# Performance work log

Measured on AMD Instinct MI355X. Metric: run time of the kernel, lower is better.

The kernel has to match this reference:

```python
import jax, jax.numpy as jnp
import numpy as np

B, S, D = 8, 2048, 512
H, LAT, OUT = 8, 64, 64


def setup_inputs() -> dict:
    key = jax.random.key(0)
    ks = jax.random.split(key, 5)
    return {
        "x": jax.random.normal(ks[0], (B, S, D), dtype=jnp.float32),
        "WQ": jax.random.normal(ks[1], (H, D, LAT), dtype=jnp.float32) * 0.05,
        "WK": jax.random.normal(ks[2], (H, D, LAT), dtype=jnp.float32) * 0.05,
        "WV": jax.random.normal(ks[3], (H, D, OUT), dtype=jnp.float32) * 0.05,
        "WO": jax.random.normal(ks[4], (H * OUT, OUT), dtype=jnp.float32) * 0.05,
    }


def reference(x, WQ, WK, WV, WO):
    # Per-head projections, vectorized over heads (faithful to the TF python loop).
    Q = jnp.einsum('bsd,hdk->bhsk', x, WQ)   # [B,H,S,LAT]
    K = jnp.einsum('bsd,hdk->bhsk', x, WK)   # [B,H,S,LAT]
    V = jnp.einsum('bsd,hdo->bhso', x, WV)   # [B,H,S,OUT]
    scale = jnp.asarray(1.0 / np.sqrt(LAT), dtype=x.dtype)
    A = jnp.einsum('bhqk,bhsk->bhqs', Q, K) * scale  # [B,H,S,S]
    A = jax.nn.softmax(A, axis=-1)
    O = jnp.einsum('bhqs,bhso->bhqo', A, V)  # [B,H,S,OUT]
    # concat heads along last axis (head 0 first, matching the TF loop order)
    O = jnp.transpose(O, (0, 2, 1, 3)).reshape(x.shape[0], x.shape[1], H * OUT)
    return O @ WO  # [B,S,OUT]
```

## Files before the change

kernel.cpp:

```cpp
#include <hip/hip_runtime.h>
#include <hip/hip_bf16.h>
#include <math.h>

static constexpr int Bn = 8, Sn = 2048, Dn = 512, Hn = 8, LATn = 64, OUTn = 64;

typedef short  bf16x8 __attribute__((ext_vector_type(8)));
typedef float  f32x4  __attribute__((ext_vector_type(4)));

__device__ __forceinline__ unsigned short f2bf(float f) {
    union { float f; unsigned int i; } v; v.f = f;
    unsigned int x = v.i;
    return (unsigned short)((x + 0x7FFFu + ((x >> 16) & 1u)) >> 16);
}
__device__ __forceinline__ unsigned int pack2bf(float a, float b) {
    unsigned int ua = __float_as_uint(a) + 0x8000u;
    unsigned int ub = __float_as_uint(b) + 0x8000u;
    return (ua >> 16) | (ub & 0xFFFF0000u);
}
__device__ __forceinline__ unsigned int cvtpk(float a, float b) {
    unsigned int r;
    asm("v_cvt_pk_bf16_f32 %0, %1, %2" : "=v"(r) : "v"(a), "v"(b));
    return r;
}

#if __has_builtin(__builtin_amdgcn_exp2f)
#define EXP2(x) __builtin_amdgcn_exp2f(x)
#else
#define EXP2(x) exp2f(x)
#endif

__device__ __forceinline__ void gl_lds16(const void* g, void* l) {
    __builtin_amdgcn_global_load_lds(
        (const __attribute__((address_space(1))) unsigned int*)g,
        (__attribute__((address_space(3))) unsigned int*)l, 16, 0, 0);
}

__global__ __launch_bounds__(256) void wprep(
    const float* __restrict__ WQ, const float* __restrict__ WK,
    const float* __restrict__ WV, const float* __restrict__ WO,
    unsigned short* __restrict__ WT)
{
    __shared__ float tile[64][65];
    const int t  = threadIdx.x;
    const int d0 = blockIdx.x * 64;
    const int yy = blockIdx.y;

    const float* W; float scale = 1.0f; size_t dstbase;
    if (yy < 24) {
        int h = yy / 3, which = yy % 3;
        W = (which == 0) ? WQ : (which == 1) ? WK : WV;
        W += (size_t)h * Dn * 64;
        if (which == 0) scale = 0.125f * 1.44269504088896f;
        dstbase = ((size_t)h * 192 + which * 64) * Dn;
    } else {
        W = WO;
        dstbase = (size_t)8 * 192 * Dn;
    }

    for (int i = 0; i < 4; ++i) {
        int idx = i * 256 + t;
        int r = idx >> 4, c = (idx & 15) * 4;
        float4 u = *(const float4*)(W + (size_t)(d0 + r) * 64 + c);
        tile[r][c] = u.x; tile[r][c+1] = u.y; tile[r][c+2] = u.z; tile[r][c+3] = u.w;
    }
    __syncthreads();
    const int n = t & 63, dd = t >> 6;
    unsigned short pk[16];
    for (int i = 0; i < 16; ++i) pk[i] = f2bf(tile[dd*16 + i][n] * scale);
    size_t dst = dstbase + (size_t)n * Dn + d0 + dd * 16;
    *(bf16x8*)(WT + dst)     = *(bf16x8*)(pk);
    *(bf16x8*)(WT + dst + 8) = *(bf16x8*)(pk + 8);
}

__global__ __launch_bounds__(256) void qkv_mfma(
    const float* __restrict__ x, const unsigned short* __restrict__ WT,
    unsigned short* __restrict__ Qb, unsigned short* __restrict__ Kb,
    unsigned short* __restrict__ VT)
{
    __shared__ __align__(16) unsigned short lds[64*72 + 192*72];
    unsigned short* Xs = lds;
    unsigned short* Ws = lds + 64*72;
    unsigned short* L  = lds;

    const int t  = threadIdx.x;
    const int w  = t >> 6, ln = t & 63;
    const int nl = ln & 15, g = ln >> 4;
    const int bh = blockIdx.y, b = bh >> 3, h = bh & 7;
    const int s0 = blockIdx.x * 64;

    f32x4 acc[4][3];
    for (int m = 0; m < 4; ++m)
        for (int j = 0; j < 3; ++j) acc[m][j] = (f32x4){0.f, 0.f, 0.f, 0.f};

    for (int k0 = 0; k0 < Dn; k0 += 64) {
        __syncthreads();
        for (int i = 0; i < 2; ++i) {
            int idx = i * 256 + t;
            int r = idx >> 3, c = (idx & 7) * 8;
            const float* src = x + ((size_t)(b * Sn + s0 + r)) * Dn + k0 + c;
            float4 u0 = *(const float4*)(src);
            float4 u1 = *(const float4*)(src + 4);
            unsigned int pk[4] = { pack2bf(u0.x, u0.y), pack2bf(u0.z, u0.w),
                                   pack2bf(u1.x, u1.y), pack2bf(u1.z, u1.w) };
            *(bf16x8*)(Xs + r*72 + c) = *(bf16x8*)pk;
        }
        for (int i = 0; i < 6; ++i) {
            int idx = i * 256 + t;
            int r = idx >> 3, c = (idx & 7) * 8;
            *(bf16x8*)(Ws + r*72 + c) =
                *(const bf16x8*)(WT + ((size_t)h * 192 + r) * Dn + k0 + c);
        }
        __syncthreads();
        #pragma unroll
        for (int kc = 0; kc < 2; ++kc) {
            bf16x8 a[4], bb[3];
            for (int m = 0; m < 4; ++m)
                a[m]  = *(const bf16x8*)(Xs + (16*m + nl)*72 + 32*kc + 8*g);
            for (int j = 0; j < 3; ++j)
                bb[j] = *(const bf16x8*)(Ws + ((3*w + j)*16 + nl)*72 + 32*kc + 8*g);
            for (int m = 0; m < 4; ++m)
                for (int j = 0; j < 3; ++j)
                    acc[m][j] = __builtin_amdgcn_mfma_f32_16x16x32_bf16(
                                    a[m], bb[j], acc[m][j], 0, 0, 0);
        }
    }
    __syncthreads();
    for (int m = 0; m < 4; ++m)
        for (int j = 0; j < 3; ++j) {
            int n = 48*w + 16*j + nl;
            for (int r = 0; r < 4; ++r)
                L[(16*m + 4*g + r)*200 + n] = f2bf(acc[m][j][r]);
        }
    __syncthreads();
    for (int i = 0; i < 4; ++i) {
        int idx = i * 256 + t;
        int r = idx >> 4, c = (idx & 15) * 8;
        bf16x8 v = *(const bf16x8*)(L + r*200 + c);
        size_t o = ((size_t)bh * Sn + s0 + r) * 64;
        if (c < 64) *(bf16x8*)(Qb + o + c)      = v;
        else        *(bf16x8*)(Kb + o + c - 64) = v;
    }
    {
        int o = t & 63, cc = t >> 6;
        unsigned short pk[16];
        for (int i = 0; i < 16; ++i) {
            int srow = 32*(cc>>1) + 16*((i>>2)&1) + 8*(cc&1) + 4*((i>>3)&1) + (i&3);
            pk[i] = L[srow*200 + 128 + o];
        }
        size_t dst = ((size_t)bh * 64 + o) * Sn + s0 + 16*cc;
        *(bf16x8*)(VT + dst)     = *(bf16x8*)(pk);
        *(bf16x8*)(VT + dst + 8) = *(bf16x8*)(pk + 8);
    }
}

__global__ __launch_bounds__(256, 2) void flash_mfma(
    const unsigned short* __restrict__ Qb,
    const unsigned short* __restrict__ Kb,
    const unsigned short* __restrict__ VT,
    unsigned short* __restrict__ Ob)
{
    __shared__ __align__(16) unsigned short KV[3][2][4096];

    const int t  = threadIdx.x;
    const int w  = t >> 6, ln = t & 63;
    const int qh = ln & 15, g = (ln >> 4) & 3;
    const int bh = blockIdx.y, b = bh >> 3, h = bh & 7;
    const int q0 = blockIdx.x * 256;
    const int qw = q0 + 64 * w;

    bf16x8 bq[4][2];
    #pragma unroll
    for (int qs = 0; qs < 4; ++qs) {
        const unsigned short* qp =
            Qb + ((size_t)bh * Sn + qw + 16*qs + qh) * 64 + 8*g;
        bq[qs][0] = *(const bf16x8*)(qp);
        bq[qs][1] = *(const bf16x8*)(qp + 32);
    }

    const int r0a = t >> 3;
    const int csa = (t & 7) ^ (r0a & 7);
    const int r0b = 32 + (t >> 3);
    const int csb = (t & 7) ^ (r0b & 7);
    const unsigned short* kga = Kb + ((size_t)bh * Sn + r0a) * 64 + csa * 8;
    const unsigned short* kgb = Kb + ((size_t)bh * Sn + r0b) * 64 + csb * 8;
    const unsigned short* vga = VT + ((size_t)bh * 64 + r0a) * Sn + csa * 8;
    const unsigned short* vgb = VT + ((size_t)bh * 64 + r0b) * Sn + csb * 8;

    const int koff0 = qh*64 + (((g    ) ^ (qh & 7)) * 8);
    const int koff1 = qh*64 + (((4 + g) ^ (qh & 7)) * 8);

    f32x4 o_acc[4][4];
    #pragma unroll
    for (int qs = 0; qs < 4; ++qs)
        #pragma unroll
        for (int f = 0; f < 4; ++f) o_acc[qs][f] = (f32x4){0.f, 0.f, 0.f, 0.f};
    float l_run[4] = {0.f, 0.f, 0.f, 0.f};

    gl_lds16(kga,        &KV[0][0][w * 512]);
    gl_lds16(kgb,        &KV[0][0][2048 + w * 512]);
    gl_lds16(vga,        &KV[0][1][w * 512]);
    gl_lds16(vgb,        &KV[0][1][2048 + w * 512]);
    gl_lds16(kga + 4096, &KV[1][0][w * 512]);
    gl_lds16(kgb + 4096, &KV[1][0][2048 + w * 512]);
    gl_lds16(vga + 64,   &KV[1][1][w * 512]);
    gl_lds16(vgb + 64,   &KV[1][1][2048 + w * 512]);

    constexpr int NT = Sn / 64;
    int buf = 0, sbuf = 2;
    for (int kt = 0; kt < NT; ++kt) {
        if (kt < NT - 1) asm volatile("s_waitcnt vmcnt(4)" ::: "memory");
        else             asm volatile("s_waitcnt vmcnt(0)" ::: "memory");
        __builtin_amdgcn_s_barrier();

        if (kt < NT - 2) {
            const size_t ko = (size_t)(kt + 2) * 4096;
            const int    vo = (kt + 2) * 64;
            gl_lds16(kga + ko, &KV[sbuf][0][w * 512]);
            gl_lds16(kgb + ko, &KV[sbuf][0][2048 + w * 512]);
            gl_lds16(vga + vo, &KV[sbuf][1][w * 512]);
            gl_lds16(vgb + vo, &KV[sbuf][1][2048 + w * 512]);
        }
        const unsigned short* Kt = KV[buf][0];
        const unsigned short* Vt = KV[buf][1];

        f32x4 st[4][4];
        #pragma unroll
        for (int qs = 0; qs < 4; ++qs)
            #pragma unroll
            for (int f = 0; f < 4; ++f) st[qs][f] = (f32x4){0.f, 0.f, 0.f, 0.f};
        __builtin_amdgcn_s_setprio(1);
        #pragma unroll
        for (int kc = 0; kc < 2; ++kc) {
            const int ko = kc ? koff1 : koff0;
            bf16x8 a0 = *(const bf16x8*)(Kt + ko);
            bf16x8 a1 = *(const bf16x8*)(Kt + ko + 1024);
            bf16x8 a2 = *(const bf16x8*)(Kt + ko + 2048);
            bf16x8 a3 = *(const bf16x8*)(Kt + ko + 3072);
            #pragma unroll
            for (int qs = 0; qs < 4; ++qs) {
                st[qs][0] = __builtin_amdgcn_mfma_f32_16x16x32_bf16(a0, bq[qs][kc], st[qs][0], 0, 0, 0);
                st[qs][1] = __builtin_amdgcn_mfma_f32_16x16x32_bf16(a1, bq[qs][kc], st[qs][1], 0, 0, 0);
                st[qs][2] = __builtin_amdgcn_mfma_f32_16x16x32_bf16(a2, bq[qs][kc], st[qs][2], 0, 0, 0);
                st[qs][3] = __builtin_amdgcn_mfma_f32_16x16x32_bf16(a3, bq[qs][kc], st[qs][3], 0, 0, 0);
            }
        }
        __builtin_amdgcn_s_setprio(0);

        bf16x8 bp[4][2];
        #pragma unroll
        for (int qs = 0; qs < 4; ++qs) {
            float e0[4], e1[4], e2[4], e3[4];
            #pragma unroll
            for (int r = 0; r < 4; ++r) {
                e0[r] = EXP2(st[qs][0][r]);
                e1[r] = EXP2(st[qs][1][r]);
                e2[r] = EXP2(st[qs][2][r]);
                e3[r] = EXP2(st[qs][3][r]);
            }
            l_run[qs] += ((e0[0]+e0[1])+(e0[2]+e0[3])) + ((e1[0]+e1[1])+(e1[2]+e1[3]))
                       + ((e2[0]+e2[1])+(e2[2]+e2[3])) + ((e3[0]+e3[1])+(e3[2]+e3[3]));
            unsigned int p0[4] = { cvtpk(e0[0],e0[1]), cvtpk(e0[2],e0[3]),
                                   cvtpk(e1[0],e1[1]), cvtpk(e1[2],e1[3]) };
            unsigned int p1[4] = { cvtpk(e2[0],e2[1]), cvtpk(e2[2],e2[3]),
                                   cvtpk(e3[0],e3[1]), cvtpk(e3[2],e3[3]) };
            bp[qs][0] = *(bf16x8*)p0;
            bp[qs][1] = *(bf16x8*)p1;
        }

        __builtin_amdgcn_s_setprio(1);
        #pragma unroll
        for (int kc = 0; kc < 2; ++kc) {
            const int ko = kc ? koff1 : koff0;
            bf16x8 v0 = *(const bf16x8*)(Vt + ko);
            bf16x8 v1 = *(const bf16x8*)(Vt + ko + 1024);
            bf16x8 v2 = *(const bf16x8*)(Vt + ko + 2048);
            bf16x8 v3 = *(const bf16x8*)(Vt + ko + 3072);
            #pragma unroll
            for (int qs = 0; qs < 4; ++qs) {
                o_acc[qs][0] = __builtin_amdgcn_mfma_f32_16x16x32_bf16(v0, bp[qs][kc], o_acc[qs][0], 0, 0, 0);
                o_acc[qs][1] = __builtin_amdgcn_mfma_f32_16x16x32_bf16(v1, bp[qs][kc], o_acc[qs][1], 0, 0, 0);
                o_acc[qs][2] = __builtin_amdgcn_mfma_f32_16x16x32_bf16(v2, bp[qs][kc], o_acc[qs][2], 0, 0, 0);
                o_acc[qs][3] = __builtin_amdgcn_mfma_f32_16x16x32_bf16(v3, bp[qs][kc], o_acc[qs][3], 0, 0, 0);
            }
        }
        __builtin_amdgcn_s_setprio(0);

        buf  = (buf  == 2) ? 0 : buf  + 1;
        sbuf = (sbuf == 2) ? 0 : sbuf + 1;
    }

    #pragma unroll
    for (int qs = 0; qs < 4; ++qs) {
        l_run[qs] += __shfl_xor(l_run[qs], 16);
        l_run[qs] += __shfl_xor(l_run[qs], 32);
    }

    #pragma unroll
    for (int qs = 0; qs < 4; ++qs) {
        float inv_l = 1.f / l_run[qs];
        unsigned short* op = Ob
            + ((size_t)(b * Sn + q0 + 64*w + 16*qs + qh)) * 512 + h*64 + 4*g;
        #pragma unroll
        for (int f = 0; f < 4; ++f) {
            unsigned int lo = cvtpk(o_acc[qs][f][0] * inv_l, o_acc[qs][f][1] * inv_l);
            unsigned int hi = cvtpk(o_acc[qs][f][2] * inv_l, o_acc[qs][f][3] * inv_l);
            *(uint2*)(op + 16*f) = make_uint2(lo, hi);
        }
    }
}

__global__ __launch_bounds__(256) void out_mfma(
    const unsigned short* __restrict__ Ob, const unsigned short* __restrict__ WOT,
    float* __restrict__ out)
{
    __shared__ __align__(16) unsigned short As[64 * 72];
    __shared__ __align__(16) unsigned short Bs[64 * 72];

    const int t  = threadIdx.x;
    const int w  = t >> 6, ln = t & 63;
    const int qh = ln & 15, g = ln >> 4;
    const int bs0 = blockIdx.x * 64;

    f32x4 acc[4];
    for (int n = 0; n < 4; ++n) acc[n] = (f32x4){0.f, 0.f, 0.f, 0.f};

    for (int k0 = 0; k0 < 512; k0 += 64) {
        __syncthreads();
        for (int i = 0; i < 2; ++i) {
            int idx = i * 256 + t;
            int r = idx >> 3, c = (idx & 7) * 8;
            *(bf16x8*)(As + r*72 + c) =
                *(const bf16x8*)(Ob + ((size_t)(bs0 + r)) * 512 + k0 + c);
            *(bf16x8*)(Bs + r*72 + c) =
                *(const bf16x8*)(WOT + (size_t)r * Dn + k0 + c);
        }
        __syncthreads();
        #pragma unroll
        for (int kc = 0; kc < 2; ++kc) {
            bf16x8 a = *(const bf16x8*)(As + (16*w + qh)*72 + 32*kc + 8*g);
            #pragma unroll
            for (int n = 0; n < 4; ++n) {
                bf16x8 bb = *(const bf16x8*)(Bs + (16*n + qh)*72 + 32*kc + 8*g);
                acc[n] = __builtin_amdgcn_mfma_f32_16x16x32_bf16(a, bb, acc[n], 0, 0, 0);
            }
        }
    }
    for (int n = 0; n < 4; ++n)
        for (int r = 0; r < 4; ++r)
            out[((size_t)(bs0 + 16*w + 4*g + r)) * 64 + 16*n + qh] = acc[n][r];
}

extern "C" void kernel_launch(void* const* d_in, const int* in_sizes, int n_in,
                              void* d_out, int out_size, void* d_ws, size_t ws_size,
                              hipStream_t stream)
{
    const float* x  = (const float*)d_in[0];
    const float* WQ = (const float*)d_in[1];
    const float* WK = (const float*)d_in[2];
    const float* WV = (const float*)d_in[3];
    const float* WO = (const float*)d_in[4];
    float* out = (float*)d_out;

    const size_t NQ = (size_t)Bn * Hn * Sn * LATn;
    char* p = (char*)d_ws;
    unsigned short* Qb  = (unsigned short*)p;           p += NQ * 2;
    unsigned short* Kb  = (unsigned short*)p;           p += NQ * 2;
    unsigned short* VT  = (unsigned short*)p;           p += NQ * 2;
    unsigned short* WT  = (unsigned short*)p;           p += ((size_t)Hn*192*Dn + 64*Dn) * 2;
    unsigned short* Ob  = (unsigned short*)p;
    unsigned short* WOT = WT + (size_t)Hn * 192 * Dn;

    wprep     <<<dim3(8, 25),         256, 0, stream>>>(WQ, WK, WV, WO, WT);
    qkv_mfma  <<<dim3(Sn/64, Bn*Hn),  256, 0, stream>>>(x, WT, Qb, Kb, VT);
    flash_mfma<<<dim3(Sn/256, Bn*Hn), 256, 0, stream>>>(Qb, Kb, VT, Ob);
    out_mfma  <<<dim3(Bn*Sn/64),      256, 0, stream>>>(Ob, WOT, out);
}
```

Baseline: 208.4 us.

## Split flash attention block into 8 waves of 32 query rows each

The flash attention kernel now launches 512 threads per block instead of 256, and each wave handles 32 query rows instead of 64. The block still covers 256 queries. Each thread now issues one K and one V global-to-LDS load per tile rather than two of each, and the waitcnt values are adjusted to match. The intent is to lower per-wave register pressure and raise the number of resident waves for better latency hiding. In exchange, each wave reuses every LDS K/V fragment read across fewer MFMAs, and barrier synchronisation now spans more waves.

```diff
diff --git a/kernel.cpp b/kernel.cpp
--- a/kernel.cpp
+++ b/kernel.cpp
@@ -153,7 +153,7 @@
     }
 }
 
-__global__ __launch_bounds__(256, 2) void flash_mfma(
+__global__ __launch_bounds__(512, 4) void flash_mfma(
     const unsigned short* __restrict__ Qb,
     const unsigned short* __restrict__ Kb,
     const unsigned short* __restrict__ VT,
@@ -166,66 +166,54 @@
     const int qh = ln & 15, g = (ln >> 4) & 3;
     const int bh = blockIdx.y, b = bh >> 3, h = bh & 7;
     const int q0 = blockIdx.x * 256;
-    const int qw = q0 + 64 * w;
-
-    bf16x8 bq[4][2];
+    const int qw = q0 + 32 * w;
+
+    bf16x8 bq[2][2];
     #pragma unroll
-    for (int qs = 0; qs < 4; ++qs) {
+    for (int qs = 0; qs < 2; ++qs) {
         const unsigned short* qp =
             Qb + ((size_t)bh * Sn + qw + 16*qs + qh) * 64 + 8*g;
         bq[qs][0] = *(const bf16x8*)(qp);
         bq[qs][1] = *(const bf16x8*)(qp + 32);
     }
 
-    const int r0a = t >> 3;
-    const int csa = (t & 7) ^ (r0a & 7);
-    const int r0b = 32 + (t >> 3);
-    const int csb = (t & 7) ^ (r0b & 7);
-    const unsigned short* kga = Kb + ((size_t)bh * Sn + r0a) * 64 + csa * 8;
-    const unsigned short* kgb = Kb + ((size_t)bh * Sn + r0b) * 64 + csb * 8;
-    const unsigned short* vga = VT + ((size_t)bh * 64 + r0a) * Sn + csa * 8;
-    const unsigned short* vgb = VT + ((size_t)bh * 64 + r0b) * Sn + csb * 8;
+    const int r0 = t >> 3;
+    const int cs = (t & 7) ^ (r0 & 7);
+    const unsigned short* kg = Kb + ((size_t)bh * Sn + r0) * 64 + cs * 8;
+    const unsigned short* vg = VT + ((size_t)bh * 64 + r0) * Sn + cs * 8;
 
     const int koff0 = qh*64 + (((g    ) ^ (qh & 7)) * 8);
     const int koff1 = qh*64 + (((4 + g) ^ (qh & 7)) * 8);
 
-    f32x4 o_acc[4][4];
+    f32x4 o_acc[2][4];
     #pragma unroll
-    for (int qs = 0; qs < 4; ++qs)
+    for (int qs = 0; qs < 2; ++qs)
         #pragma unroll
         for (int f = 0; f < 4; ++f) o_acc[qs][f] = (f32x4){0.f, 0.f, 0.f, 0.f};
-    float l_run[4] = {0.f, 0.f, 0.f, 0.f};
-
-    gl_lds16(kga,        &KV[0][0][w * 512]);
-    gl_lds16(kgb,        &KV[0][0][2048 + w * 512]);
-    gl_lds16(vga,        &KV[0][1][w * 512]);
-    gl_lds16(vgb,        &KV[0][1][2048 + w * 512]);
-    gl_lds16(kga + 4096, &KV[1][0][w * 512]);
-    gl_lds16(kgb + 4096, &KV[1][0][2048 + w * 512]);
-    gl_lds16(vga + 64,   &KV[1][1][w * 512]);
-    gl_lds16(vgb + 64,   &KV[1][1][2048 + w * 512]);
+    float l_run[2] = {0.f, 0.f};
+
+    gl_lds16(kg,        &KV[0][0][w * 512]);
+    gl_lds16(vg,        &KV[0][1][w * 512]);
+    gl_lds16(kg + 4096, &KV[1][0][w * 512]);
+    gl_lds16(vg + 64,   &KV[1][1][w * 512]);
 
     constexpr int NT = Sn / 64;
     int buf = 0, sbuf = 2;
     for (int kt = 0; kt < NT; ++kt) {
-        if (kt < NT - 1) asm volatile("s_waitcnt vmcnt(4)" ::: "memory");
+        if (kt < NT - 1) asm volatile("s_waitcnt vmcnt(2)" ::: "memory");
         else             asm volatile("s_waitcnt vmcnt(0)" ::: "memory");
         __builtin_amdgcn_s_barrier();
 
         if (kt < NT - 2) {
-            const size_t ko = (size_t)(kt + 2) * 4096;
-            const int    vo = (kt + 2) * 64;
-            gl_lds16(kga + ko, &KV[sbuf][0][w * 512]);
-            gl_lds16(kgb + ko, &KV[sbuf][0][2048 + w * 512]);
-            gl_lds16(vga + vo, &KV[sbuf][1][w * 512]);
-            gl_lds16(vgb + vo, &KV[sbuf][1][2048 + w * 512]);
+            gl_lds16(kg + (size_t)(kt + 2) * 4096, &KV[sbuf][0][w * 512]);
+            gl_lds16(vg + (size_t)(kt + 2) * 64,   &KV[sbuf][1][w * 512]);
         }
         const unsigned short* Kt = KV[buf][0];
         const unsigned short* Vt = KV[buf][1];
 
-        f32x4 st[4][4];
-        #pragma unroll
-        for (int qs = 0; qs < 4; ++qs)
+        f32x4 st[2][4];
+        #pragma unroll
+        for (int qs = 0; qs < 2; ++qs)
             #pragma unroll
             for (int f = 0; f < 4; ++f) st[qs][f] = (f32x4){0.f, 0.f, 0.f, 0.f};
         __builtin_amdgcn_s_setprio(1);
@@ -237,7 +225,7 @@
             bf16x8 a2 = *(const bf16x8*)(Kt + ko + 2048);
             bf16x8 a3 = *(const bf16x8*)(Kt + ko + 3072);
             #pragma unroll
-            for (int qs = 0; qs < 4; ++qs) {
+            for (int qs = 0; qs < 2; ++qs) {
                 st[qs][0] = __builtin_amdgcn_mfma_f32_16x16x32_bf16(a0, bq[qs][kc], st[qs][0], 0, 0, 0);
                 st[qs][1] = __builtin_amdgcn_mfma_f32_16x16x32_bf16(a1, bq[qs][kc], st[qs][1], 0, 0, 0);
                 st[qs][2] = __builtin_amdgcn_mfma_f32_16x16x32_bf16(a2, bq[qs][kc], st[qs][2], 0, 0, 0);
@@ -246,9 +234,9 @@
         }
         __builtin_amdgcn_s_setprio(0);
 
-        bf16x8 bp[4][2];
-        #pragma unroll
-        for (int qs = 0; qs < 4; ++qs) {
+        bf16x8 bp[2][2];
+        #pragma unroll
+        for (int qs = 0; qs < 2; ++qs) {
             float e0[4], e1[4], e2[4], e3[4];
             #pragma unroll
             for (int r = 0; r < 4; ++r) {
@@ -276,7 +264,7 @@
             bf16x8 v2 = *(const bf16x8*)(Vt + ko + 2048);
             bf16x8 v3 = *(const bf16x8*)(Vt + ko + 3072);
             #pragma unroll
-            for (int qs = 0; qs < 4; ++qs) {
+            for (int qs = 0; qs < 2; ++qs) {
                 o_acc[qs][0] = __builtin_amdgcn_mfma_f32_16x16x32_bf16(v0, bp[qs][kc], o_acc[qs][0], 0, 0, 0);
                 o_acc[qs][1] = __builtin_amdgcn_mfma_f32_16x16x32_bf16(v1, bp[qs][kc], o_acc[qs][1], 0, 0, 0);
                 o_acc[qs][2] = __builtin_amdgcn_mfma_f32_16x16x32_bf16(v2, bp[qs][kc], o_acc[qs][2], 0, 0, 0);
@@ -290,16 +278,16 @@
     }
 
     #pragma unroll
-    for (int qs = 0; qs < 4; ++qs) {
+    for (int qs = 0; qs < 2; ++qs) {
         l_run[qs] += __shfl_xor(l_run[qs], 16);
         l_run[qs] += __shfl_xor(l_run[qs], 32);
     }
 
     #pragma unroll
-    for (int qs = 0; qs < 4; ++qs) {
+    for (int qs = 0; qs < 2; ++qs) {
         float inv_l = 1.f / l_run[qs];
         unsigned short* op = Ob
-            + ((size_t)(b * Sn + q0 + 64*w + 16*qs + qh)) * 512 + h*64 + 4*g;
+            + ((size_t)(b * Sn + q0 + 32*w + 16*qs + qh)) * 512 + h*64 + 4*g;
         #pragma unroll
         for (int f = 0; f < 4; ++f) {
             unsigned int lo = cvtpk(o_acc[qs][f][0] * inv_l, o_acc[qs][f][1] * inv_l);
@@ -372,6 +360,6 @@
 
     wprep     <<<dim3(8, 25),         256, 0, stream>>>(WQ, WK, WV, WO, WT);
     qkv_mfma  <<<dim3(Sn/64, Bn*Hn),  256, 0, stream>>>(x, WT, Qb, Kb, VT);
-    flash_mfma<<<dim3(Sn/256, Bn*Hn), 256, 0, stream>>>(Qb, Kb, VT, Ob);
+    flash_mfma<<<dim3(Sn/256, Bn*Hn), 512, 0, stream>>>(Qb, Kb, VT, Ob);
     out_mfma  <<<dim3(Bn*Sn/64),      256, 0, stream>>>(Ob, WOT, out);
 }
```

Result: no change. 205.5 us, median of 2 (-1.4%).
